# Kernel optimization log

Measured on AMD Instinct MI355X. Metric: run time of the kernel, lower is better.

## Reference

```python
import jax, jax.numpy as jnp
import numpy as np

NB = 4          # batch size (len(unique(batch_ixs)))
NA = 1048576    # anchors per batch element
C_FG = 2        # foreground classes (probs has C_FG+1 columns)
K = 6000        # pre-NMS top-k, hard-coded in source
PATCH = (256, 256, 128)


def setup_inputs():
    key = jax.random.key(0)
    k1, k2, k3 = jax.random.split(key, 3)
    H, W, D = PATCH
    scale = jnp.array([H, W, H, W, D, D], jnp.float32)
    anchors = jax.random.uniform(k1, (NA, 6), jnp.float32) * scale   # (y1,x1,y2,x2,z1,z2) in pixel coords
    probs = jax.nn.softmax(jax.random.normal(k2, (NB * NA, C_FG + 1), jnp.float32), axis=-1)
    deltas = jax.random.normal(k3, (NB * NA, 6), jnp.float32) * 0.1
    batch_ixs = jnp.repeat(jnp.arange(NB, dtype=jnp.int32), NA)
    return {"anchors": anchors, "probs": probs, "deltas": deltas, "batch_ixs": batch_ixs}


def _refine(anchors, probs, deltas, batch_ixs):
    H, W, D = PATCH
    scale = jnp.array([H, W, H, W, D, D], jnp.float32)
    std = jnp.array([0.1, 0.1, 0.1, 0.2, 0.2, 0.2], jnp.float32)
    anchors_rep = jnp.tile(anchors, (NB, 1))            # anchors.repeat(len(unique(batch_ixs)), 1)
    fg = probs[:, 1:]                                   # (N, C_FG)
    # flat descending sort + [:6000]  ==  top_k over the flat view
    top_s, top_i = jax.lax.top_k(fg.reshape(-1), K)
    prop = top_i // C_FG                                # proposal index
    cls = top_i % C_FG + 1                              # pred class id (1-based)
    b_ix = batch_ixs[prop]
    anc = jnp.floor(anchors_rep[prop] / scale)          # torch.div(..., rounding_mode='floor')
    dlt = deltas[prop] * std
    # apply_box_deltas_3D
    h = anc[:, 2] - anc[:, 0]
    w = anc[:, 3] - anc[:, 1]
    d = anc[:, 5] - anc[:, 4]
    cy = anc[:, 0] + 0.5 * h + dlt[:, 0] * h
    cx = anc[:, 1] + 0.5 * w + dlt[:, 1] * w
    cz = anc[:, 4] + 0.5 * d + dlt[:, 2] * d
    h = h * jnp.exp(dlt[:, 3])
    w = w * jnp.exp(dlt[:, 4])
    d = d * jnp.exp(dlt[:, 5])
    y1 = cy - 0.5 * h
    x1 = cx - 0.5 * w
    z1 = cz - 0.5 * d
    boxes = jnp.stack([y1, x1, y1 + h, x1 + w, z1, z1 + d], axis=1) * scale
    hi = jnp.array([H, W, H, W, D, D], jnp.float32)
    rois = jnp.round(jnp.clip(boxes, 0.0, hi))          # clip_to_window + round -> pre_nms_rois

    # per-(batch, class) selection, replicating the source's `order[order[:2]]` double indexing
    def select(b, c):
        mask = (b_ix == b) & (cls == c)
        lp = (jnp.cumsum(mask) - 1).astype(jnp.int32)   # local position within class subset (valid where mask)
        ms = jnp.where(mask, top_s, -jnp.inf)
        ord_full = jnp.argsort(-ms)                     # local rank r -> global candidate index
        order_arr = lp[ord_full]                        # local rank r -> local position  (== torch `order`)
        q = order_arr[order_arr[:2]]                    # order[order[:2]]
        idx_src = jnp.where(mask, lp, K)                # K is out-of-range -> dropped
        sub_glob = jnp.zeros((K,), jnp.int32).at[idx_src].set(jnp.arange(K, dtype=jnp.int32), mode="drop")
        return sub_glob[q]                              # global indices of the 2 kept candidates

    pb = jnp.repeat(jnp.arange(NB, dtype=jnp.int32), C_FG)
    pc = jnp.tile(jnp.arange(1, C_FG + 1, dtype=jnp.int32), NB)
    sel = jax.vmap(select)(pb, pc)                      # (NB*C_FG, 2)
    # unique1d sorts its input; per-(b,c) subsets are disjoint so union == sort of all picks.
    # per-batch top-30 cap never binds (only C_FG*2 = 4 picks per batch).
    keep = jnp.sort(sel.reshape(-1))
    result = jnp.concatenate(
        [rois[keep],
         b_ix[keep, None].astype(jnp.float32),
         cls[keep, None].astype(jnp.float32),
         top_s[keep, None]],
        axis=1)                                         # (NB*C_FG*2, 9)
    return result


def reference(anchors, probs, deltas, batch_ixs):
    return _refine(anchors, probs, deltas, batch_ixs)
```

## Files before the change

### kernel.cpp

```cpp
#include <hip/hip_runtime.h>
#include <float.h>
#include <math.h>

#define NA_LOG2 20
#define NB_ 4
#define ROWS (NB_ << NA_LOG2)
#define B1 1024
#define T1 256
#define F4_PER_BLOCK 3072
#define F4_PER_THREAD (F4_PER_BLOCK / T1)
#define BLOCKS_PER_BATCH (B1 / NB_)

typedef unsigned long long u64;
typedef unsigned int u32;


__device__ __forceinline__ void upd2(u64& ka, u64& kb, u64 k) {
    const bool b1 = k > ka;
    const bool b2 = k > kb;
    kb = b1 ? ka : (b2 ? k : kb);
    ka = b1 ? k : ka;
}

__device__ __forceinline__ void mrg2(u64& a1, u64& a2, u64 b1, u64 b2) {
    const bool t = b1 > a1;
    const u64 n1 = t ? b1 : a1;
    const u64 c1 = t ? a1 : b1;
    const u64 c2 = t ? b2 : a2;
    a2 = (c1 > c2) ? c1 : c2;
    a1 = n1;
}

__global__ __launch_bounds__(T1) void scan_pass1(const float4* __restrict__ p4,
                                                 u64* __restrict__ wsK)
{
    const int tid = threadIdx.x;
    const int bb  = blockIdx.x;
    const int base = bb * F4_PER_BLOCK;

    u64 k1a = 0, k1b = 0, k2a = 0, k2b = 0;

#pragma unroll
    for (int k = 0; k < F4_PER_THREAD; ++k) {
        const int u = base + k * T1 + tid;
        const float4 v = p4[u];
        const int fi0 = u * 4;
        const int r0  = fi0 / 3;
        const int ph  = fi0 - r0 * 3;
#pragma unroll
        for (int j = 0; j < 4; ++j) {
            const float s = (j == 0) ? v.x : (j == 1) ? v.y : (j == 2) ? v.z : v.w;
            const int  cj   = ph + j;
            const bool wrap = (cj >= 3);
            const int  col  = wrap ? cj - 3 : cj;
            const int  row  = r0 + (wrap ? 1 : 0);
            const int  fg   = 2 * row + (col - 1);
            const u64  key  = ((u64)__float_as_uint(s) << 32) | (u32)~(u32)fg;
            upd2(k1a, k1b, (col == 1) ? key : 0ull);
            upd2(k2a, k2b, (col == 2) ? key : 0ull);
        }
    }

#pragma unroll
    for (int m = 1; m < 64; m <<= 1) {
        u64 o1 = (u64)__shfl_xor((long long)k1a, m);
        u64 o2 = (u64)__shfl_xor((long long)k1b, m);
        mrg2(k1a, k1b, o1, o2);
        o1 = (u64)__shfl_xor((long long)k2a, m);
        o2 = (u64)__shfl_xor((long long)k2b, m);
        mrg2(k2a, k2b, o1, o2);
    }

    __shared__ u64 ls[4][4];
    const int wave = tid >> 6, lane = tid & 63;
    if (lane == 0) {
        ls[wave][0] = k1a; ls[wave][1] = k1b;
        ls[wave][2] = k2a; ls[wave][3] = k2b;
    }
    __syncthreads();
    if (tid == 0) {
        for (int wv = 1; wv < 4; ++wv) {
            mrg2(k1a, k1b, ls[wv][0], ls[wv][1]);
            mrg2(k2a, k2b, ls[wv][2], ls[wv][3]);
        }
        u64* o = wsK + bb * 4;
        o[0] = k1a; o[1] = k1b; o[2] = k2a; o[3] = k2b;
    }
}

__global__ __launch_bounds__(512) void finish_pass2(const u64* __restrict__ wsK,
                                                    const float* __restrict__ anchors,
                                                    const float* __restrict__ deltas,
                                                    float* __restrict__ out)
{
    __shared__ u64 g_k[16];
    const int tid = threadIdx.x;
    const int wave = tid >> 6, lane = tid & 63;
    const int batch = wave >> 1, clsbit = wave & 1;

    u64 ka = 0, kb = 0;
#pragma unroll
    for (int j = 0; j < (2 * BLOCKS_PER_BATCH) / 64; ++j) {
        const int q   = j * 64 + lane;
        const int blk = batch * BLOCKS_PER_BATCH + (q >> 1);
        const int e   = q & 1;
        upd2(ka, kb, wsK[blk * 4 + clsbit * 2 + e]);
    }
#pragma unroll
    for (int m = 1; m < 64; m <<= 1) {
        u64 o1 = (u64)__shfl_xor((long long)ka, m);
        u64 o2 = (u64)__shfl_xor((long long)kb, m);
        mrg2(ka, kb, o1, o2);
    }
    if (lane == 0) {
        g_k[wave * 2 + 0] = ka;
        g_k[wave * 2 + 1] = kb;
    }
    __syncthreads();

    if (tid == 0) {
        for (int a = 1; a < 16; ++a) {
            const u64 kv = g_k[a];
            int b = a - 1;
            while (b >= 0 && kv > g_k[b]) { g_k[b + 1] = g_k[b]; --b; }
            g_k[b + 1] = kv;
        }
    }
    __syncthreads();

    if (tid < 16) {
        const float scale[6] = {256.f, 256.f, 256.f, 256.f, 128.f, 128.f};
        const float stdv[6]  = {0.1f, 0.1f, 0.1f, 0.2f, 0.2f, 0.2f};
        const u64 key = g_k[tid];
        const float score = __uint_as_float((u32)(key >> 32));
        const int flat = (int)~(u32)key;
        const int prop = flat >> 1;
        const int cls  = (flat & 1) + 1;
        const int b    = prop >> NA_LOG2;
        const int ar   = prop & ((1 << NA_LOG2) - 1);

        float anc[6], dlt[6];
#pragma unroll
        for (int k = 0; k < 6; ++k) {
            anc[k] = floorf(anchors[ar * 6 + k] / scale[k]);
            dlt[k] = deltas[prop * 6 + k] * stdv[k];
        }
        float h = anc[2] - anc[0];
        float w = anc[3] - anc[1];
        float d = anc[5] - anc[4];
        float cy = anc[0] + 0.5f * h + dlt[0] * h;
        float cx = anc[1] + 0.5f * w + dlt[1] * w;
        float cz = anc[4] + 0.5f * d + dlt[2] * d;
        h *= expf(dlt[3]);
        w *= expf(dlt[4]);
        d *= expf(dlt[5]);
        const float y1 = cy - 0.5f * h, x1 = cx - 0.5f * w, z1 = cz - 0.5f * d;
        const float box[6] = {y1, x1, y1 + h, x1 + w, z1, z1 + d};

        float* o = out + tid * 9;
#pragma unroll
        for (int k = 0; k < 6; ++k) {
            float bx = box[k] * scale[k];
            bx = fminf(fmaxf(bx, 0.f), scale[k]);
            o[k] = rintf(bx);
        }
        o[6] = (float)b;
        o[7] = (float)cls;
        o[8] = score;
    }
}

extern "C" void kernel_launch(void* const* d_in, const int* in_sizes, int n_in,
                              void* d_out, int out_size, void* d_ws, size_t ws_size,
                              hipStream_t stream)
{
    const float* anchors = (const float*)d_in[0];
    const float* probs   = (const float*)d_in[1];
    const float* deltas  = (const float*)d_in[2];

    u64* wsK = (u64*)d_ws;

    scan_pass1<<<dim3(B1), dim3(T1), 0, stream>>>((const float4*)probs, wsK);
    finish_pass2<<<dim3(1), dim3(512), 0, stream>>>(wsK, anchors, deltas, (float*)d_out);
}
```

Before: 185.0 us.

## Stage probs through LDS with async global_load_lds and unrolled fixed column pattern

Each block copies a 24KB chunk of the probs array into shared memory using direct global-to-LDS loads. Threads then process 4-row segments, reading three float4s each with a fixed column pattern. This removes the per-element division by 3 and the wrap logic. The grid doubles to 2048 blocks. The change trades extra LDS usage and a barrier for cheaper index arithmetic and more loads in flight.

```diff
diff --git a/kernel.cpp b/kernel.cpp
--- a/kernel.cpp
+++ b/kernel.cpp
@@ -4,11 +4,12 @@
 
 #define NA_LOG2 20
 #define NB_ 4
-#define ROWS (NB_ << NA_LOG2)
-#define B1 1024
+#define B1 2048
 #define T1 256
-#define F4_PER_BLOCK 3072
-#define F4_PER_THREAD (F4_PER_BLOCK / T1)
+#define BYTES_PER_BLOCK 24576
+#define CHUNKS 6
+#define SEGS 512
+#define SEGS_PER_THREAD 2
 #define BLOCKS_PER_BATCH (B1 / NB_)
 
 typedef unsigned long long u64;
@@ -31,34 +32,45 @@
     a1 = n1;
 }
 
-__global__ __launch_bounds__(T1) void scan_pass1(const float4* __restrict__ p4,
+__global__ __launch_bounds__(T1) void scan_pass1(const char* __restrict__ probs,
                                                  u64* __restrict__ wsK)
 {
+    __shared__ __align__(16) char smem[BYTES_PER_BLOCK];
+    __shared__ u64 ls[4][4];
+
     const int tid = threadIdx.x;
     const int bb  = blockIdx.x;
-    const int base = bb * F4_PER_BLOCK;
+    const char* gbase = probs + (size_t)bb * BYTES_PER_BLOCK;
 
+#pragma unroll
+    for (int c = 0; c < CHUNKS; ++c) {
+        const int off = (c * T1 + tid) * 16;
+        __builtin_amdgcn_global_load_lds(
+            (const __attribute__((address_space(1))) void*)(gbase + off),
+            (__attribute__((address_space(3))) void*)(smem + off),
+            16, 0, 0);
+    }
+    __syncthreads();
+
+    const float4* sm4 = (const float4*)smem;
     u64 k1a = 0, k1b = 0, k2a = 0, k2b = 0;
 
 #pragma unroll
-    for (int k = 0; k < F4_PER_THREAD; ++k) {
-        const int u = base + k * T1 + tid;
-        const float4 v = p4[u];
-        const int fi0 = u * 4;
-        const int r0  = fi0 / 3;
-        const int ph  = fi0 - r0 * 3;
-#pragma unroll
-        for (int j = 0; j < 4; ++j) {
-            const float s = (j == 0) ? v.x : (j == 1) ? v.y : (j == 2) ? v.z : v.w;
-            const int  cj   = ph + j;
-            const bool wrap = (cj >= 3);
-            const int  col  = wrap ? cj - 3 : cj;
-            const int  row  = r0 + (wrap ? 1 : 0);
-            const int  fg   = 2 * row + (col - 1);
-            const u64  key  = ((u64)__float_as_uint(s) << 32) | (u32)~(u32)fg;
-            upd2(k1a, k1b, (col == 1) ? key : 0ull);
-            upd2(k2a, k2b, (col == 2) ? key : 0ull);
-        }
+    for (int k = 0; k < SEGS_PER_THREAD; ++k) {
+        const int seg = k * T1 + tid;
+        const float4 a = sm4[seg * 3 + 0];
+        const float4 b = sm4[seg * 3 + 1];
+        const float4 c = sm4[seg * 3 + 2];
+        const u32 f0  = ((u32)(bb * SEGS + seg)) * 8;
+        const u32 nf0 = ~f0;
+        upd2(k1a, k1b, ((u64)__float_as_uint(a.y) << 32) | (u64)(nf0 - 0));
+        upd2(k2a, k2b, ((u64)__float_as_uint(a.z) << 32) | (u64)(nf0 - 1));
+        upd2(k1a, k1b, ((u64)__float_as_uint(b.x) << 32) | (u64)(nf0 - 2));
+        upd2(k2a, k2b, ((u64)__float_as_uint(b.y) << 32) | (u64)(nf0 - 3));
+        upd2(k1a, k1b, ((u64)__float_as_uint(b.w) << 32) | (u64)(nf0 - 4));
+        upd2(k2a, k2b, ((u64)__float_as_uint(c.x) << 32) | (u64)(nf0 - 5));
+        upd2(k1a, k1b, ((u64)__float_as_uint(c.z) << 32) | (u64)(nf0 - 6));
+        upd2(k2a, k2b, ((u64)__float_as_uint(c.w) << 32) | (u64)(nf0 - 7));
     }
 
 #pragma unroll
@@ -71,7 +83,6 @@
         mrg2(k2a, k2b, o1, o2);
     }
 
-    __shared__ u64 ls[4][4];
     const int wave = tid >> 6, lane = tid & 63;
     if (lane == 0) {
         ls[wave][0] = k1a; ls[wave][1] = k1b;
@@ -180,6 +191,6 @@
 
     u64* wsK = (u64*)d_ws;
 
-    scan_pass1<<<dim3(B1), dim3(T1), 0, stream>>>((const float4*)probs, wsK);
+    scan_pass1<<<dim3(B1), dim3(T1), 0, stream>>>((const char*)probs, wsK);
     finish_pass2<<<dim3(1), dim3(512), 0, stream>>>(wsK, anchors, deltas, (float*)d_out);
 }
```

New measurement: 184.1 us. No clear change (-0.5%).
